# Kernel optimization log

Hardware: AMD Instinct MI355X
Metric: run time of the kernel (lower is better)

The kernel has to match this reference:

```python
import jax, jax.numpy as jnp
import numpy as np

EPS = 1e-6          # module eps for denominator
KERNEL_EPS = 1e-4   # performer softmax_kernel numerical eps


def softmax_kernel(data, projection):
    # data: [n, l, h, e]; projection: [m, e] -> features [n, l, h, m]
    d = data.shape[-1]
    m = projection.shape[0]
    data_normalizer = d ** -0.25
    ratio = m ** -0.5
    data_dash = jnp.einsum('nlhe,me->nlhm', data * data_normalizer, projection)
    diag_data = (0.5 * (data_normalizer ** 2)) * jnp.sum(data * data, axis=-1, keepdims=True)
    # numerically stable exp with per-row max subtraction
    data_dash = ratio * (jnp.exp(data_dash - diag_data - jnp.max(data_dash, axis=-1, keepdims=True)) + KERNEL_EPS)
    return data_dash


def _gaussian_orthogonal_random_matrix(nb_rows, nb_cols, seed=0):
    rng = np.random.default_rng(seed)
    blocks = []
    for _ in range(int(np.ceil(nb_rows / nb_cols))):
        q, _ = np.linalg.qr(rng.standard_normal((nb_cols, nb_cols)))
        blocks.append(q.T)
    proj = np.concatenate(blocks, axis=0)[:nb_rows]
    # scaling=0: chi-distributed row multipliers
    multiplier = np.linalg.norm(rng.standard_normal((nb_rows, nb_cols)), axis=1)
    return (multiplier[:, None] * proj).astype(np.float32)


def setup_inputs() -> dict:
    n, l, h, e = 2, 2048, 8, 64
    nb_features = l  # module: nb_features = l when l >= e
    key = jax.random.key(0)
    kq, kk, kv = jax.random.split(key, 3)
    queries = jax.random.normal(kq, (n, l, h, e), jnp.float32)
    keys = jax.random.normal(kk, (n, l, h, e), jnp.float32)
    values = jax.random.normal(kv, (n, l, h, e), jnp.float32)
    projection = jnp.asarray(_gaussian_orthogonal_random_matrix(nb_features, e))
    return {"queries": queries, "keys": keys, "values": values, "projection": projection}


def reference(queries, keys, values, projection):
    # Performer linear attention, batched (bi=None) branch
    q = softmax_kernel(queries, projection)   # [n, l, h, m]
    k = softmax_kernel(keys, projection)      # [n, l, h, m]
    kv = jnp.einsum('nshm,nshe->nhem', k, values)              # [n, h, e, m]
    z = 1.0 / (jnp.einsum('nlhm,nhm->nlh', q, k.sum(axis=1)) + EPS)  # [n, l, h]
    v = jnp.einsum('nlhm,nhem,nlh->nlhe', q, kv, z)             # [n, l, h, e]
    return v
```

## Files before the change

kernel.cpp:

```cpp
#include <hip/hip_runtime.h>


#define LL 2048
#define HH 8
#define MM 2048
#define ROWSTR 512

#define NORMC 0.35355339059327373f
#define LOG2E 1.4426950408889634f
#define NORMC2 (NORMC * LOG2E)
#define RATIO 0.022097086912079608f
#define KEPS 1e-4f
#define REPS (RATIO * KEPS)
#define EPSD 1e-6f

#define KVSPLIT 2097152
#define RSPLIT 32768

typedef __attribute__((ext_vector_type(8))) short short8;
typedef __attribute__((ext_vector_type(16))) float f32x16;

#define MFMA32(a, b, c) __builtin_amdgcn_mfma_f32_32x32x16_bf16((a), (b), (c), 0, 0, 0)

__device__ __forceinline__ void wg_barrier_lds() {
    asm volatile("s_waitcnt lgkmcnt(0)" ::: "memory");
    __builtin_amdgcn_s_barrier();
    __builtin_amdgcn_sched_barrier(0);
}

__device__ __forceinline__ f32x16 zero16() {
    f32x16 v;
    #pragma unroll
    for (int i = 0; i < 16; ++i) v[i] = 0.f;
    return v;
}
__device__ __forceinline__ unsigned short f2bf(float f) {
    union { float f; unsigned int u; } v; v.f = f;
    unsigned int r = v.u + 0x7fffu + ((v.u >> 16) & 1u);
    return (unsigned short)(r >> 16);
}
__device__ __forceinline__ unsigned int pk2(float lo, float hi) {
    return __builtin_amdgcn_perm(__float_as_uint(hi), __float_as_uint(lo), 0x07060302u);
}
__device__ __forceinline__ float bf2f(unsigned short u) {
    union { unsigned int ui; float f; } v; v.ui = ((unsigned int)u) << 16; return v.f;
}

template <bool BF16>
__device__ __forceinline__ short8 row_load8(const void* src, size_t rowbase, int off) {
    if (BF16) {
        return *(const short8*)((const unsigned short*)src + rowbase + off);
    } else {
        const float* p = (const float*)src + rowbase + off;
        float4 f0 = ((const float4*)p)[0], f1 = ((const float4*)p)[1];
        union { unsigned int u[4]; short8 s; } v;
        v.u[0] = pk2(f0.x, f0.y); v.u[1] = pk2(f0.z, f0.w);
        v.u[2] = pk2(f1.x, f1.y); v.u[3] = pk2(f1.z, f1.w);
        return v.s;
    }
}

template <bool BF16>
__device__ __forceinline__ void tile_load(const void* src, size_t base, size_t rstride,
                                          int t, uint4& A, uint4& B) {
    const int row = t >> 2, c16 = (t & 3) * 16;
    if (BF16) {
        const unsigned short* p = (const unsigned short*)src + base + (size_t)row * rstride + c16;
        A = *(const uint4*)p;
        B = *(const uint4*)(p + 8);
    } else {
        const float* p = (const float*)src + base + (size_t)row * rstride + c16;
        float4 f0 = ((const float4*)p)[0], f1 = ((const float4*)p)[1];
        float4 f2 = ((const float4*)p)[2], f3 = ((const float4*)p)[3];
        A.x = pk2(f0.x, f0.y); A.y = pk2(f0.z, f0.w);
        A.z = pk2(f1.x, f1.y); A.w = pk2(f1.z, f1.w);
        B.x = pk2(f2.x, f2.y); B.y = pk2(f2.z, f2.w);
        B.z = pk2(f3.x, f3.y); B.w = pk2(f3.z, f3.w);
    }
}
__device__ __forceinline__ void tile_store72(unsigned short* D, int t, uint4 A, uint4 B) {
    const int row = t >> 2, c16 = (t & 3) * 16;
    *(uint4*)&D[row * 72 + c16] = A;
    *(uint4*)&D[row * 72 + c16 + 8] = B;
}

template <bool BF16>
__device__ __forceinline__ void vt_load(const void* V, size_t base, int t, uint4& A, uint4& B) {
    const int s0 = (t & 31) * 2, e0 = (t >> 5) * 8;
    if (BF16) {
        const unsigned short* p = (const unsigned short*)V + base + (size_t)s0 * ROWSTR + e0;
        A = *(const uint4*)p;
        B = *(const uint4*)(p + ROWSTR);
    } else {
        const float* p = (const float*)V + base + (size_t)s0 * ROWSTR + e0;
        float4 f0 = ((const float4*)p)[0], f1 = ((const float4*)p)[1];
        const float* q = p + ROWSTR;
        float4 g0 = ((const float4*)q)[0], g1 = ((const float4*)q)[1];
        A.x = pk2(f0.x, f0.y); A.y = pk2(f0.z, f0.w);
        A.z = pk2(f1.x, f1.y); A.w = pk2(f1.z, f1.w);
        B.x = pk2(g0.x, g0.y); B.y = pk2(g0.z, g0.w);
        B.z = pk2(g1.x, g1.y); B.w = pk2(g1.z, g1.w);
    }
}
__device__ __forceinline__ void vt_store72(unsigned short* VT, int t, uint4 A, uint4 B) {
    const int s0 = (t & 31) * 2, e0 = (t >> 5) * 8;
    const unsigned ua[4] = {A.x, A.y, A.z, A.w}, ub[4] = {B.x, B.y, B.z, B.w};
    #pragma unroll
    for (int i = 0; i < 4; ++i) {
        *(unsigned*)&VT[(e0 + 2 * i) * 72 + s0] = (ua[i] & 0xFFFFu) | (ub[i] << 16);
        *(unsigned*)&VT[(e0 + 2 * i + 1) * 72 + s0] = (ua[i] >> 16) | (ub[i] & 0xFFFF0000u);
    }
}

__device__ __forceinline__ short8 xfrag(const unsigned int pd[8], int cp, int hi) {
    const unsigned int s0 = hi ? pd[4 * cp + 0] : pd[4 * cp + 2];
    const unsigned int s1 = hi ? pd[4 * cp + 1] : pd[4 * cp + 3];
    const unsigned int r0 = (unsigned int)__shfl_xor((int)s0, 32);
    const unsigned int r1 = (unsigned int)__shfl_xor((int)s1, 32);
    union { unsigned int u[4]; short8 s; } v;
    v.u[0] = hi ? r0 : pd[4 * cp + 0];
    v.u[1] = hi ? r1 : pd[4 * cp + 1];
    v.u[2] = hi ? pd[4 * cp + 2] : r0;
    v.u[3] = hi ? pd[4 * cp + 3] : r1;
    return v.s;
}

__global__ void LinearAttention_15985868276494_detect(const unsigned short* __restrict__ P,
                                                      float* __restrict__ flag) {
    if (threadIdx.x == 0) {
        int sane = 1;
        #pragma unroll
        for (int i = 0; i < 16; ++i) {
            const unsigned e = (P[2 * i] >> 7) & 0xFF;
            if (e < 101 || e > 141) sane = 0;
        }
        *flag = sane ? 1.0f : 0.0f;
    }
}

template <bool BF16>
__device__ void stats_impl(const void* X, const void* P, float* cws, char* smem) {
    unsigned short* Ps = (unsigned short*)smem;
    float* red = (float*)(smem + 18432);
    const int t = threadIdx.x;
    const int w = t >> 6, ln = t & 31, hi = (t >> 5) & 1;
    const int mstrip = w & 1, r3 = w >> 1;
    const int row_base = blockIdx.x * 128;
    const int ph = blockIdx.x & 31;

    short8 xb[4];
    #pragma unroll
    for (int c = 0; c < 4; ++c)
        xb[c] = row_load8<BF16>(X, (size_t)(row_base + r3 * 32 + ln) * 64, 16 * c + 8 * hi);

    const bool stP = (t < 256);
    const int tl = t & 255;
    uint4 pA, pB;
    if (stP) {
        uint4 a0, b0;
        tile_load<BF16>(P, (size_t)(ph * 64) * 64, 64, tl, a0, b0);
        tile_store72(Ps, tl, a0, b0);
        tile_load<BF16>(P, (size_t)(((ph + 1) & 31) * 64) * 64, 64, tl, pA, pB);
    }
    wg_barrier_lds();

    float rmax = -3e38f;
    for (int i = 0; i < 32; ++i) {
        const int cur = i & 1;
        unsigned short* Pc = Ps + cur * 4608;
        f32x16 acc = zero16();
        #pragma unroll
        for (int c = 0; c < 4; ++c) {
            const short8 af = *(const short8*)&Pc[(32 * mstrip + ln) * 72 + 16 * c + 8 * hi];
            acc = MFMA32(af, xb[c], acc);
        }
        if (stP && i + 1 < 32) {
            tile_store72(Ps + (cur ^ 1) * 4608, tl, pA, pB);
            if (i + 2 < 32)
                tile_load<BF16>(P, (size_t)(((i + 2 + ph) & 31) * 64) * 64, 64, tl, pA, pB);
        }
        #pragma unroll
        for (int r = 0; r < 16; ++r) rmax = fmaxf(rmax, acc[r]);
        wg_barrier_lds();
    }
    rmax = fmaxf(rmax, __shfl_xor(rmax, 32));
    if (hi == 0) red[w * 32 + ln] = rmax;
    float s2 = 0.f;
    if (mstrip == 0) {
        #pragma unroll
        for (int c = 0; c < 4; ++c) {
            union { short8 s; unsigned int u[4]; } uv; uv.s = xb[c];
            #pragma unroll
            for (int i2 = 0; i2 < 4; ++i2) {
                const float lo = bf2f((unsigned short)(uv.u[i2] & 0xFFFF));
                const float hv = bf2f((unsigned short)(uv.u[i2] >> 16));
                s2 = fmaf(lo, lo, s2); s2 = fmaf(hv, hv, s2);
            }
        }
        s2 += __shfl_xor(s2, 32);
    }
    wg_barrier_lds();
    if (mstrip == 0 && hi == 0) {
        const float rm = fmaxf(red[w * 32 + ln], red[(w + 1) * 32 + ln]);
        const int rg = row_base + r3 * 32 + ln;
        const int n = rg >> 14, l = (rg >> 3) & 2047, h = rg & 7;
        cws[(size_t)((n << 3) | h) * LL + l] =
            (NORMC * rm + (0.5f * NORMC * NORMC) * s2) * LOG2E;
    }
}

__global__ __launch_bounds__(512, 4) void LinearAttention_15985868276494_stats(
        const void* K, const void* Q, const void* P, const float* flag,
        float* c_k, float* c_q) {
    extern __shared__ char smem_st[];
    const void* X = (blockIdx.y == 0) ? K : Q;
    float* cws = (blockIdx.y == 0) ? c_k : c_q;
    if (*flag != 0.f) stats_impl<true>(X, P, cws, smem_st);
    else stats_impl<false>(X, P, cws, smem_st);
}

template <bool BF16>
__device__ void kv_impl(const void* K, const void* V, const void* P, const float* cws,
                        float* kvf01, float* ksum01, char* smem) {
    unsigned short* Ks = (unsigned short*)smem;
    unsigned short* VT = (unsigned short*)(smem + 18432);
    float* cks = (float*)(smem + 36864);

    const int t = threadIdx.x;
    const int w = t >> 6, ln = t & 31, hi = (t >> 5) & 1;
    const int mc = w;
    const int bid = blockIdx.x;
    const int xcd = bid & 7, rr = bid >> 3;
    const int gq = rr >> 3, mtb = rr & 7;
    const int g = gq * 8 + xcd;
    const int nh = g >> 2, sp = g & 3;
    const int n = nh >> 3, h = nh & 7;
    const size_t xbase = (size_t)n * (LL * ROWSTR) + (size_t)h * 64;
    const int st0 = sp * 8;
    const int mbase = mtb * 256;
    const int ph = mtb & 7;

    const bool stK = (t < 256);
    const int tl = t & 255;

    short8 pb[4];
    #pragma unroll
    for (int c = 0; c < 4; ++c)
        pb[c] = row_load8<BF16>(P, (size_t)(mbase + mc * 32 + ln) * 64, 16 * c + 8 * hi);

    uint4 kA, kB, vA, vB; float ckr = 0.f;
    {
        const int s_a = st0 + ph, s_b = st0 + ((ph + 1) & 7);
        if (stK) {
            tile_load<BF16>(K, xbase + (size_t)(s_a * 64) * ROWSTR, ROWSTR, tl, kA, kB);
            tile_store72(Ks, tl, kA, kB);
            tile_load<BF16>(K, xbase + (size_t)(s_b * 64) * ROWSTR, ROWSTR, tl, kA, kB);
        } else {
            vt_load<BF16>(V, xbase + (size_t)(s_a * 64) * ROWSTR, tl, vA, vB);
            vt_store72(VT, tl, vA, vB);
            vt_load<BF16>(V, xbase + (size_t)(s_b * 64) * ROWSTR, tl, vA, vB);
        }
        if (t < 64) {
            cks[t] = cws[(size_t)nh * LL + s_a * 64 + t];
            ckr = cws[(size_t)nh * LL + s_b * 64 + t];
        }
    }
    wg_barrier_lds();

    f32x16 akv0 = zero16(), akv1 = zero16();
    float ks = 0.f;

    for (int i = 0; i < 8; ++i) {
        const int cur = i & 1;
        unsigned short* Kc = Ks + cur * 4608;
        unsigned short* Vc = VT + cur * 4608;
        const float* cc = cks + cur * 64;
        #pragma unroll
        for (int ss = 0; ss < 2; ++ss) {
            f32x16 D = zero16();
            #pragma unroll
            for (int c = 0; c < 4; ++c) {
                const short8 af = *(const short8*)&Kc[(32 * ss + ln) * 72 + 16 * c + 8 * hi];
                D = MFMA32(af, pb[c], D);
            }
            if (ss == 0 && i + 1 < 8) {
                if (stK) tile_store72(Ks + (cur ^ 1) * 4608, tl, kA, kB);
                else vt_store72(VT + (cur ^ 1) * 4608, tl, vA, vB);
                if (t < 64) cks[(cur ^ 1) * 64 + t] = ckr;
                if (i + 2 < 8) {
                    const int st = st0 + ((i + 2 + ph) & 7);
                    if (stK) tile_load<BF16>(K, xbase + (size_t)(st * 64) * ROWSTR, ROWSTR, tl, kA, kB);
                    else vt_load<BF16>(V, xbase + (size_t)(st * 64) * ROWSTR, tl, vA, vB);
                    if (t < 64) ckr = cws[(size_t)nh * LL + st * 64 + t];
                }
            }
            unsigned int pd[8];
            #pragma unroll
            for (int gIdx = 0; gIdx < 4; ++gIdx) {
                const float4 c4 = *(const float4*)&cc[32 * ss + 8 * gIdx + 4 * hi];
                const float ca[4] = {c4.x, c4.y, c4.z, c4.w};
                float f[4];
                #pragma unroll
                for (int b = 0; b < 4; ++b) {
                    const float arg = fminf(fmaf(D[4 * gIdx + b], NORMC2, -ca[b]), 0.f);
                    f[b] = fmaf(__builtin_amdgcn_exp2f(arg), RATIO, REPS);
                }
                ks += (f[0] + f[1]) + (f[2] + f[3]);
                pd[2 * gIdx] = pk2(f[0], f[1]);
                pd[2 * gIdx + 1] = pk2(f[2], f[3]);
            }
            #pragma unroll
            for (int cp = 0; cp < 2; ++cp) {
                const short8 bf = xfrag(pd, cp, hi);
                const int scol = 32 * ss + 16 * cp + 8 * hi;
                const short8 v0 = *(const short8*)&Vc[ln * 72 + scol];
                const short8 v1 = *(const short8*)&Vc[(32 + ln) * 72 + scol];
                akv0 = MFMA32(v0, bf, akv0);
                akv1 = MFMA32(v1, bf, akv1);
            }
        }
        wg_barrier_lds();
    }
    {
        ks += __shfl_xor(ks, 32);
        const int m = mbase + mc * 32 + ln;
        if (hi == 0)
            ksum01[(size_t)sp * RSPLIT + (size_t)nh * MM + m] = ks;
        float* basep = kvf01 + (size_t)sp * KVSPLIT + (size_t)nh * (size_t)(64 * MM) + m;
        #pragma unroll
        for (int r = 0; r < 16; ++r) {
            const int e = (r & 3) + 8 * (r >> 2) + 4 * hi;
            basep[(size_t)e * MM] = akv0[r];
            basep[(size_t)(e + 32) * MM] = akv1[r];
        }
    }
}

__global__ __launch_bounds__(512, 4) void LinearAttention_15985868276494_kv(
        const void* K, const void* V, const void* P, const float* flag,
        const float* cws, float* kvf01, float* ksum01) {
    extern __shared__ char smem_kv[];
    if (*flag != 0.f) kv_impl<true>(K, V, P, cws, kvf01, ksum01, smem_kv);
    else kv_impl<false>(K, V, P, cws, kvf01, ksum01, smem_kv);
}

__global__ __launch_bounds__(256) void LinearAttention_15985868276494_reduce(
        const float* __restrict__ kvf01, const float* __restrict__ ksum01,
        unsigned short* __restrict__ kvT, float* __restrict__ ksumW) {
    const int gid = blockIdx.x * 256 + threadIdx.x;
    const size_t i4 = (size_t)gid * 4;
    const float4 a = *(const float4*)&kvf01[i4];
    const float4 b = *(const float4*)&kvf01[KVSPLIT + i4];
    const float4 c = *(const float4*)&kvf01[2 * (size_t)KVSPLIT + i4];
    const float4 d = *(const float4*)&kvf01[3 * (size_t)KVSPLIT + i4];
    uint2 o;
    o.x = (unsigned)f2bf(a.x + b.x + c.x + d.x) | ((unsigned)f2bf(a.y + b.y + c.y + d.y) << 16);
    o.y = (unsigned)f2bf(a.z + b.z + c.z + d.z) | ((unsigned)f2bf(a.w + b.w + c.w + d.w) << 16);
    *(uint2*)&kvT[i4] = o;
    if (blockIdx.x < 32) {
        const float4 e = *(const float4*)&ksum01[i4];
        const float4 f = *(const float4*)&ksum01[RSPLIT + i4];
        const float4 g = *(const float4*)&ksum01[2 * RSPLIT + i4];
        const float4 h = *(const float4*)&ksum01[3 * RSPLIT + i4];
        *(float4*)&ksumW[i4] = make_float4(e.x + f.x + g.x + h.x, e.y + f.y + g.y + h.y,
                                           e.z + f.z + g.z + h.z, e.w + f.w + g.w + h.w);
    }
}

template <bool BF16>
__device__ void out_impl(const void* Q, const void* P, const float* cqw,
                         const unsigned short* kvT, const float* ksum,
                         float* po, float* pad, char* smem) {
    unsigned short* Ps = (unsigned short*)smem;
    unsigned short* KVs = (unsigned short*)(smem + 18432);
    unsigned short* kss = (unsigned short*)(smem + 36864);
    float* fin = (float*)smem;

    const int t = threadIdx.x;
    const int w = t >> 6, ln = t & 31, hi = (t >> 5) & 1;
    const int lc = w & 3, mspl = w >> 2;
    const int bid = blockIdx.x;
    const int xcd = bid & 7, rr = bid >> 3;
    const int gq = rr >> 4, lbb = rr & 15;
    const int g = gq * 8 + xcd;
    const int nh = g >> 1, sp = g & 1;
    const int n = nh >> 3, h = nh & 7;
    const size_t qbase = (size_t)n * (LL * ROWSTR) + (size_t)h * 64;
    const size_t kvbase = (size_t)nh * (size_t)(64 * MM);
    const int mt0 = sp * 16;
    const int lbase = lbb * 128;
    const int ph = lbb;

    const bool stP = (t < 256);
    const int tl = t & 255;

    short8 qb[4];
    #pragma unroll
    for (int c = 0; c < 4; ++c)
        qb[c] = row_load8<BF16>(Q, qbase + (size_t)(lbase + lc * 32 + ln) * ROWSTR, 16 * c + 8 * hi);
    const float cq = cqw[(size_t)nh * LL + lbase + lc * 32 + ln];

    uint4 pA, pB, kA, kB; float ksr = 0.f;
    {
        const int m_a = mt0 + (ph & 15), m_b = mt0 + ((ph + 1) & 15);
        if (stP) {
            tile_load<BF16>(P, (size_t)(m_a * 64) * 64, 64, tl, pA, pB);
            tile_store72(Ps, tl, pA, pB);
            tile_load<BF16>(P, (size_t)(m_b * 64) * 64, 64, tl, pA, pB);
        } else {
            tile_load<true>(kvT, kvbase + m_a * 64, MM, tl, kA, kB);
            tile_store72(KVs, tl, kA, kB);
            tile_load<true>(kvT, kvbase + m_b * 64, MM, tl, kA, kB);
        }
        if (t < 64) {
            kss[t] = f2bf(ksum[(size_t)nh * MM + m_a * 64 + t]);
            ksr = ksum[(size_t)nh * MM + m_b * 64 + t];
        }
    }
    wg_barrier_lds();

    f32x16 ao0 = zero16(), ao1 = zero16(), ad = zero16();

    for (int i = 0; i < 16; ++i) {
        const int cur = i & 1;
        unsigned short* Pc = Ps + cur * 4608;
        unsigned short* Kc = KVs + cur * 4608;
        const unsigned short* ksc = kss + cur * 64;
        f32x16 D = zero16();
        #pragma unroll
        for (int c = 0; c < 4; ++c) {
            const short8 af = *(const short8*)&Pc[(32 * mspl + ln) * 72 + 16 * c + 8 * hi];
            D = MFMA32(af, qb[c], D);
        }
        if (i + 1 < 16) {
            if (stP) tile_store72(Ps + (cur ^ 1) * 4608, tl, pA, pB);
            else tile_store72(KVs + (cur ^ 1) * 4608, tl, kA, kB);
            if (t < 64) kss[(cur ^ 1) * 64 + t] = f2bf(ksr);
            if (i + 2 < 16) {
                const int mt = mt0 + ((i + 2 + ph) & 15);
                if (stP) tile_load<BF16>(P, (size_t)(mt * 64) * 64, 64, tl, pA, pB);
                else tile_load<true>(kvT, kvbase + mt * 64, MM, tl, kA, kB);
                if (t < 64) ksr = ksum[(size_t)nh * MM + mt * 64 + t];
            }
        }
        unsigned int pd[8];
        #pragma unroll
        for (int gIdx = 0; gIdx < 4; ++gIdx) {
            float f[4];
            #pragma unroll
            for (int b = 0; b < 4; ++b) {
                const float arg = fminf(fmaf(D[4 * gIdx + b], NORMC2, -cq), 0.f);
                f[b] = fmaf(__builtin_amdgcn_exp2f(arg), RATIO, REPS);
            }
            pd[2 * gIdx] = pk2(f[0], f[1]);
            pd[2 * gIdx + 1] = pk2(f[2], f[3]);
        }
        #pragma unroll
        for (int cp = 0; cp < 2; ++cp) {
            const short8 bf = xfrag(pd, cp, hi);
            const int mcol = 32 * mspl + 16 * cp + 8 * hi;
            const short8 a0 = *(const short8*)&Kc[ln * 72 + mcol];
            const short8 a1 = *(const short8*)&Kc[(32 + ln) * 72 + mcol];
            const short8 k8 = *(const short8*)&ksc[mcol];
            ao0 = MFMA32(a0, bf, ao0);
            ao1 = MFMA32(a1, bf, ao1);
            ad = MFMA32(k8, bf, ad);
        }
        wg_barrier_lds();
    }
    #pragma unroll 1
    for (int e2 = 0; e2 < 2; ++e2) {
        if ((lc >> 1) == e2) {
            const int slot = ((lc & 1) * 2 + mspl);
            const int addr = (slot * 64 + (t & 63)) * 33;
            #pragma unroll
            for (int r = 0; r < 16; ++r) fin[addr + r] = ao0[r];
            #pragma unroll
            for (int r = 0; r < 16; ++r) fin[addr + 16 + r] = ao1[r];
            fin[addr + 32] = ad[0];
        }
        wg_barrier_lds();
        {
            const int l64 = t >> 3, eg = t & 7;
            const int lcl = l64 >> 5, lane_l = l64 & 31;
            const int s0 = (lcl * 2) * 64, s1 = (lcl * 2 + 1) * 64;
            const float adt = fin[(s0 + lane_l) * 33 + 32] + fin[(s1 + lane_l) * 33 + 32];
            const int l = lbase + (e2 * 2 + lcl) * 32 + lane_l;
            const size_t row = (size_t)(n * LL + l) * HH + h;
            if (eg == 0) pad[(size_t)sp * RSPLIT + row] = adt;
            float* dst = po + (size_t)sp * KVSPLIT + row * 64 + eg * 8;
            #pragma unroll
            for (int jq = 0; jq < 2; ++jq) {
                float o[4];
                #pragma unroll
                for (int b = 0; b < 4; ++b) {
                    const int e = eg * 8 + 4 * jq + b;
                    const int t16 = e >> 5, e5 = e & 31;
                    const int hi_s = (e5 >> 2) & 1;
                    const int reg = 16 * t16 + (e5 & 3) + 4 * (e5 >> 3);
                    const int lane_s = hi_s * 32 + lane_l;
                    o[b] = fin[(s0 + lane_s) * 33 + reg] + fin[(s1 + lane_s) * 33 + reg];
                }
                *(float4*)&dst[4 * jq] = make_float4(o[0], o[1], o[2], o[3]);
            }
        }
        wg_barrier_lds();
    }
}

__global__ __launch_bounds__(512, 4) void LinearAttention_15985868276494_out(
        const void* Q, const void* P, const float* flag, const float* cqw,
        const unsigned short* kvT, const float* ksum, float* po, float* pad) {
    extern __shared__ char smem_out[];
    if (*flag != 0.f) out_impl<true>(Q, P, cqw, kvT, ksum, po, pad, smem_out);
    else out_impl<false>(Q, P, cqw, kvT, ksum, po, pad, smem_out);
}

__global__ __launch_bounds__(256) void LinearAttention_15985868276494_out2(
        const float* __restrict__ po, const float* __restrict__ pad,
        const float* __restrict__ flag, void* __restrict__ outp) {
    const int gid = blockIdx.x * 256 + threadIdx.x;
    const int row = gid >> 2, eg = gid & 3;
    const float adt = pad[row] + pad[RSPLIT + row];
    const float z = 1.0f / (adt + EPSD);
    const size_t base = (size_t)row * 64 + eg * 16;
    float vals[16];
    #pragma unroll
    for (int q4 = 0; q4 < 4; ++q4) {
        const float4 a = *(const float4*)&po[base + 4 * q4];
        const float4 b = *(const float4*)&po[KVSPLIT + base + 4 * q4];
        vals[4 * q4 + 0] = (a.x + b.x) * z;
        vals[4 * q4 + 1] = (a.y + b.y) * z;
        vals[4 * q4 + 2] = (a.z + b.z) * z;
        vals[4 * q4 + 3] = (a.w + b.w) * z;
    }
    if (*flag != 0.f) {
        uint4 o0, o1;
        o0.x = (unsigned)f2bf(vals[0]) | ((unsigned)f2bf(vals[1]) << 16);
        o0.y = (unsigned)f2bf(vals[2]) | ((unsigned)f2bf(vals[3]) << 16);
        o0.z = (unsigned)f2bf(vals[4]) | ((unsigned)f2bf(vals[5]) << 16);
        o0.w = (unsigned)f2bf(vals[6]) | ((unsigned)f2bf(vals[7]) << 16);
        o1.x = (unsigned)f2bf(vals[8]) | ((unsigned)f2bf(vals[9]) << 16);
        o1.y = (unsigned)f2bf(vals[10]) | ((unsigned)f2bf(vals[11]) << 16);
        o1.z = (unsigned)f2bf(vals[12]) | ((unsigned)f2bf(vals[13]) << 16);
        o1.w = (unsigned)f2bf(vals[14]) | ((unsigned)f2bf(vals[15]) << 16);
        unsigned short* op = (unsigned short*)outp + base;
        *(uint4*)op = o0;
        *(uint4*)(op + 8) = o1;
    } else {
        float* op = (float*)outp + base;
        #pragma unroll
        for (int q4 = 0; q4 < 4; ++q4)
            *(float4*)&op[4 * q4] = make_float4(vals[4 * q4], vals[4 * q4 + 1],
                                                vals[4 * q4 + 2], vals[4 * q4 + 3]);
    }
}

extern "C" void kernel_launch(void* const* d_in, const int* in_sizes, int n_in,
                              void* d_out, int out_size, void* d_ws, size_t ws_size,
                              hipStream_t stream) {
    const void* Q = d_in[0];
    const void* K = d_in[1];
    const void* V = d_in[2];
    const void* P = d_in[3];

    float* W = (float*)d_ws;
    float* flag = W;
    float* c_k = W + 16;
    float* c_q = c_k + 32768;
    float* ksum01 = c_q + 32768;
    float* kvf01 = ksum01 + 4 * RSPLIT;
    float* ksumW = kvf01 + 4 * (size_t)KVSPLIT;
    unsigned short* kvTW = (unsigned short*)(ksumW + RSPLIT);

    LinearAttention_15985868276494_detect<<<1, 64, 0, stream>>>(
        (const unsigned short*)P, flag);
    LinearAttention_15985868276494_stats<<<dim3(256, 2), 512, 19456, stream>>>(
        K, Q, P, flag, c_k, c_q);
    LinearAttention_15985868276494_kv<<<dim3(512), 512, 37376, stream>>>(
        K, V, P, flag, c_k, kvf01, ksum01);
    LinearAttention_15985868276494_reduce<<<2048, 256, 0, stream>>>(
        kvf01, ksum01, kvTW, ksumW);
    LinearAttention_15985868276494_out<<<dim3(512), 512, 37120, stream>>>(
        Q, P, flag, c_q, kvTW, ksumW, kvf01, ksum01);
    LinearAttention_15985868276494_out2<<<512, 256, 0, stream>>>(
        kvf01, ksum01, flag, d_out);
}
```

Measured before the change: 180.6 us.

## Software-pipeline the feature-projection MFMA one step ahead with triple-buffered tiles

In the kv and out kernels, the projection MFMA for the next sub-tile is now issued before the exp and second-GEMM work of the current sub-tile, so the two MFMA chains can overlap. The K and P tiles move to a three-slot LDS ring, which lets the next tile be read while the tile after it is being stored. This raises LDS use per block from about 37 KB to about 46 KB and adds live registers for the extra accumulator, which may lower occupancy.

```diff
diff --git a/kernel.cpp b/kernel.cpp
--- a/kernel.cpp
+++ b/kernel.cpp
@@ -223,8 +223,8 @@
 __device__ void kv_impl(const void* K, const void* V, const void* P, const float* cws,
                         float* kvf01, float* ksum01, char* smem) {
     unsigned short* Ks = (unsigned short*)smem;
-    unsigned short* VT = (unsigned short*)(smem + 18432);
-    float* cks = (float*)(smem + 36864);
+    unsigned short* VT = (unsigned short*)(smem + 27648);
+    float* cks = (float*)(smem + 46080);
 
     const int t = threadIdx.x;
     const int w = t >> 6, ln = t & 31, hi = (t >> 5) & 1;
@@ -250,48 +250,73 @@
 
     uint4 kA, kB, vA, vB; float ckr = 0.f;
     {
-        const int s_a = st0 + ph, s_b = st0 + ((ph + 1) & 7);
+        const int s0i = st0 + (ph & 7);
+        const int s1i = st0 + ((ph + 1) & 7);
+        const int s2i = st0 + ((ph + 2) & 7);
         if (stK) {
-            tile_load<BF16>(K, xbase + (size_t)(s_a * 64) * ROWSTR, ROWSTR, tl, kA, kB);
+            tile_load<BF16>(K, xbase + (size_t)(s0i * 64) * ROWSTR, ROWSTR, tl, kA, kB);
             tile_store72(Ks, tl, kA, kB);
-            tile_load<BF16>(K, xbase + (size_t)(s_b * 64) * ROWSTR, ROWSTR, tl, kA, kB);
+            tile_load<BF16>(K, xbase + (size_t)(s1i * 64) * ROWSTR, ROWSTR, tl, kA, kB);
+            tile_store72(Ks + 4608, tl, kA, kB);
+            tile_load<BF16>(K, xbase + (size_t)(s2i * 64) * ROWSTR, ROWSTR, tl, kA, kB);
         } else {
-            vt_load<BF16>(V, xbase + (size_t)(s_a * 64) * ROWSTR, tl, vA, vB);
+            vt_load<BF16>(V, xbase + (size_t)(s0i * 64) * ROWSTR, tl, vA, vB);
             vt_store72(VT, tl, vA, vB);
-            vt_load<BF16>(V, xbase + (size_t)(s_b * 64) * ROWSTR, tl, vA, vB);
+            vt_load<BF16>(V, xbase + (size_t)(s1i * 64) * ROWSTR, tl, vA, vB);
         }
         if (t < 64) {
-            cks[t] = cws[(size_t)nh * LL + s_a * 64 + t];
-            ckr = cws[(size_t)nh * LL + s_b * 64 + t];
+            cks[t] = cws[(size_t)nh * LL + s0i * 64 + t];
+            ckr = cws[(size_t)nh * LL + s1i * 64 + t];
         }
     }
     wg_barrier_lds();
+
+    f32x16 D = zero16();
+    #pragma unroll
+    for (int c = 0; c < 4; ++c) {
+        const short8 af = *(const short8*)&Ks[ln * 72 + 16 * c + 8 * hi];
+        D = MFMA32(af, pb[c], D);
+    }
 
     f32x16 akv0 = zero16(), akv1 = zero16();
     float ks = 0.f;
 
     for (int i = 0; i < 8; ++i) {
-        const int cur = i & 1;
-        unsigned short* Kc = Ks + cur * 4608;
-        unsigned short* Vc = VT + cur * 4608;
-        const float* cc = cks + cur * 64;
+        unsigned short* Vc = VT + (i & 1) * 4608;
+        const float* cc = cks + (i & 1) * 64;
         #pragma unroll
         for (int ss = 0; ss < 2; ++ss) {
-            f32x16 D = zero16();
-            #pragma unroll
-            for (int c = 0; c < 4; ++c) {
-                const short8 af = *(const short8*)&Kc[(32 * ss + ln) * 72 + 16 * c + 8 * hi];
-                D = MFMA32(af, pb[c], D);
+            f32x16 Dn = zero16();
+            const int jn = 2 * i + ss + 1;
+            if (jn < 16) {
+                const int tn = jn >> 1, ssn = jn & 1;
+                unsigned short* Kc = Ks + (tn % 3) * 4608;
+                #pragma unroll
+                for (int c = 0; c < 4; ++c) {
+                    const short8 af = *(const short8*)&Kc[(32 * ssn + ln) * 72 + 16 * c + 8 * hi];
+                    Dn = MFMA32(af, pb[c], Dn);
+                }
             }
             if (ss == 0 && i + 1 < 8) {
-                if (stK) tile_store72(Ks + (cur ^ 1) * 4608, tl, kA, kB);
-                else vt_store72(VT + (cur ^ 1) * 4608, tl, vA, vB);
-                if (t < 64) cks[(cur ^ 1) * 64 + t] = ckr;
-                if (i + 2 < 8) {
-                    const int st = st0 + ((i + 2 + ph) & 7);
-                    if (stK) tile_load<BF16>(K, xbase + (size_t)(st * 64) * ROWSTR, ROWSTR, tl, kA, kB);
-                    else vt_load<BF16>(V, xbase + (size_t)(st * 64) * ROWSTR, tl, vA, vB);
-                    if (t < 64) ckr = cws[(size_t)nh * LL + st * 64 + t];
+                if (stK) {
+                    if (i + 2 < 8) tile_store72(Ks + ((i + 2) % 3) * 4608, tl, kA, kB);
+                    if (i + 3 < 8) {
+                        const int st = st0 + ((i + 3 + ph) & 7);
+                        tile_load<BF16>(K, xbase + (size_t)(st * 64) * ROWSTR, ROWSTR, tl, kA, kB);
+                    }
+                } else {
+                    vt_store72(VT + ((i + 1) & 1) * 4608, tl, vA, vB);
+                    if (i + 2 < 8) {
+                        const int st = st0 + ((i + 2 + ph) & 7);
+                        vt_load<BF16>(V, xbase + (size_t)(st * 64) * ROWSTR, tl, vA, vB);
+                    }
+                }
+                if (t < 64) {
+                    cks[((i + 1) & 1) * 64 + t] = ckr;
+                    if (i + 2 < 8) {
+                        const int st = st0 + ((i + 2 + ph) & 7);
+                        ckr = cws[(size_t)nh * LL + st * 64 + t];
+                    }
                 }
             }
             unsigned int pd[8];
@@ -318,6 +343,7 @@
                 akv0 = MFMA32(v0, bf, akv0);
                 akv1 = MFMA32(v1, bf, akv1);
             }
+            D = Dn;
         }
         wg_barrier_lds();
     }
@@ -372,8 +398,8 @@
                          const unsigned short* kvT, const float* ksum,
                          float* po, float* pad, char* smem) {
     unsigned short* Ps = (unsigned short*)smem;
-    unsigned short* KVs = (unsigned short*)(smem + 18432);
-    unsigned short* kss = (unsigned short*)(smem + 36864);
+    unsigned short* KVs = (unsigned short*)(smem + 27648);
+    unsigned short* kss = (unsigned short*)(smem + 46080);
     float* fin = (float*)smem;
 
     const int t = threadIdx.x;
@@ -402,45 +428,66 @@
 
     uint4 pA, pB, kA, kB; float ksr = 0.f;
     {
-        const int m_a = mt0 + (ph & 15), m_b = mt0 + ((ph + 1) & 15);
+        const int m0i = mt0 + (ph & 15);
+        const int m1i = mt0 + ((ph + 1) & 15);
+        const int m2i = mt0 + ((ph + 2) & 15);
         if (stP) {
-            tile_load<BF16>(P, (size_t)(m_a * 64) * 64, 64, tl, pA, pB);
+            tile_load<BF16>(P, (size_t)(m0i * 64) * 64, 64, tl, pA, pB);
             tile_store72(Ps, tl, pA, pB);
-            tile_load<BF16>(P, (size_t)(m_b * 64) * 64, 64, tl, pA, pB);
+            tile_load<BF16>(P, (size_t)(m1i * 64) * 64, 64, tl, pA, pB);
+            tile_store72(Ps + 4608, tl, pA, pB);
+            tile_load<BF16>(P, (size_t)(m2i * 64) * 64, 64, tl, pA, pB);
         } else {
-            tile_load<true>(kvT, kvbase + m_a * 64, MM, tl, kA, kB);
+            tile_load<true>(kvT, kvbase + m0i * 64, MM, tl, kA, kB);
             tile_store72(KVs, tl, kA, kB);
-            tile_load<true>(kvT, kvbase + m_b * 64, MM, tl, kA, kB);
+            tile_load<true>(kvT, kvbase + m1i * 64, MM, tl, kA, kB);
         }
         if (t < 64) {
-            kss[t] = f2bf(ksum[(size_t)nh * MM + m_a * 64 + t]);
-            ksr = ksum[(size_t)nh * MM + m_b * 64 + t];
+            kss[t] = f2bf(ksum[(size_t)nh * MM + m0i * 64 + t]);
+            ksr = ksum[(size_t)nh * MM + m1i * 64 + t];
         }
     }
     wg_barrier_lds();
 
+    f32x16 D = zero16();
+    #pragma unroll
+    for (int c = 0; c < 4; ++c) {
+        const short8 af = *(const short8*)&Ps[(32 * mspl + ln) * 72 + 16 * c + 8 * hi];
+        D = MFMA32(af, qb[c], D);
+    }
+
     f32x16 ao0 = zero16(), ao1 = zero16(), ad = zero16();
 
     for (int i = 0; i < 16; ++i) {
-        const int cur = i & 1;
-        unsigned short* Pc = Ps + cur * 4608;
-        unsigned short* Kc = KVs + cur * 4608;
-        const unsigned short* ksc = kss + cur * 64;
-        f32x16 D = zero16();
-        #pragma unroll
-        for (int c = 0; c < 4; ++c) {
-            const short8 af = *(const short8*)&Pc[(32 * mspl + ln) * 72 + 16 * c + 8 * hi];
-            D = MFMA32(af, qb[c], D);
-        }
+        f32x16 Dn = zero16();
         if (i + 1 < 16) {
-            if (stP) tile_store72(Ps + (cur ^ 1) * 4608, tl, pA, pB);
-            else tile_store72(KVs + (cur ^ 1) * 4608, tl, kA, kB);
-            if (t < 64) kss[(cur ^ 1) * 64 + t] = f2bf(ksr);
-            if (i + 2 < 16) {
-                const int mt = mt0 + ((i + 2 + ph) & 15);
-                if (stP) tile_load<BF16>(P, (size_t)(mt * 64) * 64, 64, tl, pA, pB);
-                else tile_load<true>(kvT, kvbase + mt * 64, MM, tl, kA, kB);
-                if (t < 64) ksr = ksum[(size_t)nh * MM + mt * 64 + t];
+            unsigned short* Pc = Ps + ((i + 1) % 3) * 4608;
+            #pragma unroll
+            for (int c = 0; c < 4; ++c) {
+                const short8 af = *(const short8*)&Pc[(32 * mspl + ln) * 72 + 16 * c + 8 * hi];
+                Dn = MFMA32(af, qb[c], Dn);
+            }
+        }
+        if (i + 1 < 16) {
+            if (stP) {
+                if (i + 2 < 16) tile_store72(Ps + ((i + 2) % 3) * 4608, tl, pA, pB);
+                if (i + 3 < 16) {
+                    const int mt = mt0 + ((i + 3 + ph) & 15);
+                    tile_load<BF16>(P, (size_t)(mt * 64) * 64, 64, tl, pA, pB);
+                }
+            } else {
+                tile_store72(KVs + ((i + 1) & 1) * 4608, tl, kA, kB);
+                if (i + 2 < 16) {
+                    const int mt = mt0 + ((i + 2 + ph) & 15);
+                    tile_load<true>(kvT, kvbase + mt * 64, MM, tl, kA, kB);
+                }
+            }
+            if (t < 64) {
+                kss[((i + 1) & 1) * 64 + t] = f2bf(ksr);
+                if (i + 2 < 16) {
+                    const int mt = mt0 + ((i + 2 + ph) & 15);
+                    ksr = ksum[(size_t)nh * MM + mt * 64 + t];
+                }
             }
         }
         unsigned int pd[8];
@@ -455,17 +502,22 @@
             pd[2 * gIdx] = pk2(f[0], f[1]);
             pd[2 * gIdx + 1] = pk2(f[2], f[3]);
         }
-        #pragma unroll
-        for (int cp = 0; cp < 2; ++cp) {
-            const short8 bf = xfrag(pd, cp, hi);
-            const int mcol = 32 * mspl + 16 * cp + 8 * hi;
-            const short8 a0 = *(const short8*)&Kc[ln * 72 + mcol];
-            const short8 a1 = *(const short8*)&Kc[(32 + ln) * 72 + mcol];
-            const short8 k8 = *(const short8*)&ksc[mcol];
-            ao0 = MFMA32(a0, bf, ao0);
-            ao1 = MFMA32(a1, bf, ao1);
-            ad = MFMA32(k8, bf, ad);
-        }
+        {
+            unsigned short* Kc = KVs + (i & 1) * 4608;
+            const unsigned short* ksc = kss + (i & 1) * 64;
+            #pragma unroll
+            for (int cp = 0; cp < 2; ++cp) {
+                const short8 bf = xfrag(pd, cp, hi);
+                const int mcol = 32 * mspl + 16 * cp + 8 * hi;
+                const short8 a0 = *(const short8*)&Kc[ln * 72 + mcol];
+                const short8 a1 = *(const short8*)&Kc[(32 + ln) * 72 + mcol];
+                const short8 k8 = *(const short8*)&ksc[mcol];
+                ao0 = MFMA32(a0, bf, ao0);
+                ao1 = MFMA32(a1, bf, ao1);
+                ad = MFMA32(k8, bf, ad);
+            }
+        }
+        D = Dn;
         wg_barrier_lds();
     }
     #pragma unroll 1
@@ -577,11 +629,11 @@
         (const unsigned short*)P, flag);
     LinearAttention_15985868276494_stats<<<dim3(256, 2), 512, 19456, stream>>>(
         K, Q, P, flag, c_k, c_q);
-    LinearAttention_15985868276494_kv<<<dim3(512), 512, 37376, stream>>>(
+    LinearAttention_15985868276494_kv<<<dim3(512), 512, 46592, stream>>>(
         K, V, P, flag, c_k, kvf01, ksum01);
     LinearAttention_15985868276494_reduce<<<2048, 256, 0, stream>>>(
         kvf01, ksum01, kvTW, ksumW);
-    LinearAttention_15985868276494_out<<<dim3(512), 512, 37120, stream>>>(
+    LinearAttention_15985868276494_out<<<dim3(512), 512, 46336, stream>>>(
         Q, P, flag, c_q, kvTW, ksumW, kvf01, ksum01);
     LinearAttention_15985868276494_out2<<<512, 256, 0, stream>>>(
         kvf01, ksum01, flag, d_out);
```

New measurement: 205.1 us. +13.6%, slower.

## Fuse out2 normalization into out kernel by dropping the m-split

Applied to the files above, without the earlier changes.

The output kernel no longer splits the feature dimension across two blocks and writes fp32 partials. Each block now covers 64 rows of l over all 2048 features, processing two 64-wide feature tiles per iteration. Waves are split four ways across tile-half and m-half, and the partials are reduced in LDS. The normalization and bf16/fp32 store are done in-kernel, which removes the out2 launch and the partial-buffer round trip through global memory. In exchange, LDS use per block doubles to about 74 KB, which may lower occupancy, and each block does more serial work.

```diff
diff --git a/kernel.cpp b/kernel.cpp
--- a/kernel.cpp
+++ b/kernel.cpp
@@ -370,26 +370,24 @@
 template <bool BF16>
 __device__ void out_impl(const void* Q, const void* P, const float* cqw,
                          const unsigned short* kvT, const float* ksum,
-                         float* po, float* pad, char* smem) {
+                         void* outp, char* smem) {
     unsigned short* Ps = (unsigned short*)smem;
-    unsigned short* KVs = (unsigned short*)(smem + 18432);
-    unsigned short* kss = (unsigned short*)(smem + 36864);
+    unsigned short* KVs = (unsigned short*)(smem + 36864);
+    unsigned short* kss = (unsigned short*)(smem + 73728);
     float* fin = (float*)smem;
 
     const int t = threadIdx.x;
     const int w = t >> 6, ln = t & 31, hi = (t >> 5) & 1;
-    const int lc = w & 3, mspl = w >> 2;
+    const int lc = w & 1, mspl = (w >> 1) & 1, ts = w >> 2;
     const int bid = blockIdx.x;
     const int xcd = bid & 7, rr = bid >> 3;
-    const int gq = rr >> 4, lbb = rr & 15;
-    const int g = gq * 8 + xcd;
-    const int nh = g >> 1, sp = g & 1;
+    const int nh = xcd | ((rr & 1) << 3);
+    const int lbb = rr >> 1;
     const int n = nh >> 3, h = nh & 7;
     const size_t qbase = (size_t)n * (LL * ROWSTR) + (size_t)h * 64;
     const size_t kvbase = (size_t)nh * (size_t)(64 * MM);
-    const int mt0 = sp * 16;
-    const int lbase = lbb * 128;
-    const int ph = lbb;
+    const int lbase = lbb * 64;
+    const int ph = lbb & 15;
 
     const bool stP = (t < 256);
     const int tl = t & 255;
@@ -400,21 +398,27 @@
         qb[c] = row_load8<BF16>(Q, qbase + (size_t)(lbase + lc * 32 + ln) * ROWSTR, 16 * c + 8 * hi);
     const float cq = cqw[(size_t)nh * LL + lbase + lc * 32 + ln];
 
-    uint4 pA, pB, kA, kB; float ksr = 0.f;
+    uint4 eA, eB, oA, oB; float ksr = 0.f;
     {
-        const int m_a = mt0 + (ph & 15), m_b = mt0 + ((ph + 1) & 15);
+        const int p0 = ph, p1 = (ph + 1) & 15;
         if (stP) {
-            tile_load<BF16>(P, (size_t)(m_a * 64) * 64, 64, tl, pA, pB);
-            tile_store72(Ps, tl, pA, pB);
-            tile_load<BF16>(P, (size_t)(m_b * 64) * 64, 64, tl, pA, pB);
+            tile_load<BF16>(P, (size_t)(p0 * 128) * 64, 64, tl, eA, eB);
+            tile_store72(Ps, tl, eA, eB);
+            tile_load<BF16>(P, (size_t)(p0 * 128 + 64) * 64, 64, tl, eA, eB);
+            tile_store72(Ps + 4608, tl, eA, eB);
+            tile_load<BF16>(P, (size_t)(p1 * 128) * 64, 64, tl, eA, eB);
+            tile_load<BF16>(P, (size_t)(p1 * 128 + 64) * 64, 64, tl, oA, oB);
         } else {
-            tile_load<true>(kvT, kvbase + m_a * 64, MM, tl, kA, kB);
-            tile_store72(KVs, tl, kA, kB);
-            tile_load<true>(kvT, kvbase + m_b * 64, MM, tl, kA, kB);
-        }
-        if (t < 64) {
-            kss[t] = f2bf(ksum[(size_t)nh * MM + m_a * 64 + t]);
-            ksr = ksum[(size_t)nh * MM + m_b * 64 + t];
+            tile_load<true>(kvT, kvbase + p0 * 128, MM, tl, eA, eB);
+            tile_store72(KVs, tl, eA, eB);
+            tile_load<true>(kvT, kvbase + p0 * 128 + 64, MM, tl, eA, eB);
+            tile_store72(KVs + 4608, tl, eA, eB);
+            tile_load<true>(kvT, kvbase + p1 * 128, MM, tl, eA, eB);
+            tile_load<true>(kvT, kvbase + p1 * 128 + 64, MM, tl, oA, oB);
+        }
+        if (t < 128) {
+            kss[t] = f2bf(ksum[(size_t)nh * MM + p0 * 128 + t]);
+            ksr = ksum[(size_t)nh * MM + p1 * 128 + t];
         }
     }
     wg_barrier_lds();
@@ -423,9 +427,9 @@
 
     for (int i = 0; i < 16; ++i) {
         const int cur = i & 1;
-        unsigned short* Pc = Ps + cur * 4608;
-        unsigned short* Kc = KVs + cur * 4608;
-        const unsigned short* ksc = kss + cur * 64;
+        unsigned short* Pc = Ps + cur * 9216 + ts * 4608;
+        unsigned short* Kc = KVs + cur * 9216 + ts * 4608;
+        const unsigned short* ksc = kss + cur * 128 + ts * 64;
         f32x16 D = zero16();
         #pragma unroll
         for (int c = 0; c < 4; ++c) {
@@ -433,14 +437,29 @@
             D = MFMA32(af, qb[c], D);
         }
         if (i + 1 < 16) {
-            if (stP) tile_store72(Ps + (cur ^ 1) * 4608, tl, pA, pB);
-            else tile_store72(KVs + (cur ^ 1) * 4608, tl, kA, kB);
-            if (t < 64) kss[(cur ^ 1) * 64 + t] = f2bf(ksr);
-            if (i + 2 < 16) {
-                const int mt = mt0 + ((i + 2 + ph) & 15);
-                if (stP) tile_load<BF16>(P, (size_t)(mt * 64) * 64, 64, tl, pA, pB);
-                else tile_load<true>(kvT, kvbase + mt * 64, MM, tl, kA, kB);
-                if (t < 64) ksr = ksum[(size_t)nh * MM + mt * 64 + t];
+            if (stP) {
+                tile_store72(Ps + (cur ^ 1) * 9216, tl, eA, eB);
+                tile_store72(Ps + (cur ^ 1) * 9216 + 4608, tl, oA, oB);
+                if (i + 2 < 16) {
+                    const int p = (i + 2 + ph) & 15;
+                    tile_load<BF16>(P, (size_t)(p * 128) * 64, 64, tl, eA, eB);
+                    tile_load<BF16>(P, (size_t)(p * 128 + 64) * 64, 64, tl, oA, oB);
+                }
+            } else {
+                tile_store72(KVs + (cur ^ 1) * 9216, tl, eA, eB);
+                tile_store72(KVs + (cur ^ 1) * 9216 + 4608, tl, oA, oB);
+                if (i + 2 < 16) {
+                    const int p = (i + 2 + ph) & 15;
+                    tile_load<true>(kvT, kvbase + p * 128, MM, tl, eA, eB);
+                    tile_load<true>(kvT, kvbase + p * 128 + 64, MM, tl, oA, oB);
+                }
+            }
+            if (t < 128) {
+                kss[(cur ^ 1) * 128 + t] = f2bf(ksr);
+                if (i + 2 < 16) {
+                    const int p = (i + 2 + ph) & 15;
+                    ksr = ksum[(size_t)nh * MM + p * 128 + t];
+                }
             }
         }
         unsigned int pd[8];
@@ -470,9 +489,8 @@
     }
     #pragma unroll 1
     for (int e2 = 0; e2 < 2; ++e2) {
-        if ((lc >> 1) == e2) {
-            const int slot = ((lc & 1) * 2 + mspl);
-            const int addr = (slot * 64 + (t & 63)) * 33;
+        if (lc == e2) {
+            const int addr = ((mspl * 2 + ts) * 64 + (t & 63)) * 33;
             #pragma unroll
             for (int r = 0; r < 16; ++r) fin[addr + r] = ao0[r];
             #pragma unroll
@@ -481,27 +499,35 @@
         }
         wg_barrier_lds();
         {
-            const int l64 = t >> 3, eg = t & 7;
-            const int lcl = l64 >> 5, lane_l = l64 & 31;
-            const int s0 = (lcl * 2) * 64, s1 = (lcl * 2 + 1) * 64;
-            const float adt = fin[(s0 + lane_l) * 33 + 32] + fin[(s1 + lane_l) * 33 + 32];
-            const int l = lbase + (e2 * 2 + lcl) * 32 + lane_l;
+            const int l32 = t >> 4, eg = t & 15;
+            const int lane_l = l32;
+            float adt = 0.f;
+            #pragma unroll
+            for (int s = 0; s < 4; ++s) adt += fin[(s * 64 + lane_l) * 33 + 32];
+            const float z = 1.0f / (adt + EPSD);
+            const int l = lbase + e2 * 32 + l32;
             const size_t row = (size_t)(n * LL + l) * HH + h;
-            if (eg == 0) pad[(size_t)sp * RSPLIT + row] = adt;
-            float* dst = po + (size_t)sp * KVSPLIT + row * 64 + eg * 8;
-            #pragma unroll
-            for (int jq = 0; jq < 2; ++jq) {
-                float o[4];
+            float vals[4];
+            #pragma unroll
+            for (int b = 0; b < 4; ++b) {
+                const int e = eg * 4 + b;
+                const int t16 = e >> 5, e5 = e & 31;
+                const int hi_s = (e5 >> 2) & 1;
+                const int reg = 16 * t16 + (e5 & 3) + 4 * (e5 >> 3);
+                const int lane_s = hi_s * 32 + lane_l;
+                float o = 0.f;
                 #pragma unroll
-                for (int b = 0; b < 4; ++b) {
-                    const int e = eg * 8 + 4 * jq + b;
-                    const int t16 = e >> 5, e5 = e & 31;
-                    const int hi_s = (e5 >> 2) & 1;
-                    const int reg = 16 * t16 + (e5 & 3) + 4 * (e5 >> 3);
-                    const int lane_s = hi_s * 32 + lane_l;
-                    o[b] = fin[(s0 + lane_s) * 33 + reg] + fin[(s1 + lane_s) * 33 + reg];
-                }
-                *(float4*)&dst[4 * jq] = make_float4(o[0], o[1], o[2], o[3]);
+                for (int s = 0; s < 4; ++s) o += fin[(s * 64 + lane_s) * 33 + reg];
+                vals[b] = o * z;
+            }
+            if (BF16) {
+                uint2 ov;
+                ov.x = (unsigned)f2bf(vals[0]) | ((unsigned)f2bf(vals[1]) << 16);
+                ov.y = (unsigned)f2bf(vals[2]) | ((unsigned)f2bf(vals[3]) << 16);
+                *(uint2*)((unsigned short*)outp + row * 64 + eg * 4) = ov;
+            } else {
+                *(float4*)((float*)outp + row * 64 + eg * 4) =
+                    make_float4(vals[0], vals[1], vals[2], vals[3]);
             }
         }
         wg_barrier_lds();
@@ -510,50 +536,10 @@
 
 __global__ __launch_bounds__(512, 4) void LinearAttention_15985868276494_out(
         const void* Q, const void* P, const float* flag, const float* cqw,
-        const unsigned short* kvT, const float* ksum, float* po, float* pad) {
+        const unsigned short* kvT, const float* ksum, void* outp) {
     extern __shared__ char smem_out[];
-    if (*flag != 0.f) out_impl<true>(Q, P, cqw, kvT, ksum, po, pad, smem_out);
-    else out_impl<false>(Q, P, cqw, kvT, ksum, po, pad, smem_out);
-}
-
-__global__ __launch_bounds__(256) void LinearAttention_15985868276494_out2(
-        const float* __restrict__ po, const float* __restrict__ pad,
-        const float* __restrict__ flag, void* __restrict__ outp) {
-    const int gid = blockIdx.x * 256 + threadIdx.x;
-    const int row = gid >> 2, eg = gid & 3;
-    const float adt = pad[row] + pad[RSPLIT + row];
-    const float z = 1.0f / (adt + EPSD);
-    const size_t base = (size_t)row * 64 + eg * 16;
-    float vals[16];
-    #pragma unroll
-    for (int q4 = 0; q4 < 4; ++q4) {
-        const float4 a = *(const float4*)&po[base + 4 * q4];
-        const float4 b = *(const float4*)&po[KVSPLIT + base + 4 * q4];
-        vals[4 * q4 + 0] = (a.x + b.x) * z;
-        vals[4 * q4 + 1] = (a.y + b.y) * z;
-        vals[4 * q4 + 2] = (a.z + b.z) * z;
-        vals[4 * q4 + 3] = (a.w + b.w) * z;
-    }
-    if (*flag != 0.f) {
-        uint4 o0, o1;
-        o0.x = (unsigned)f2bf(vals[0]) | ((unsigned)f2bf(vals[1]) << 16);
-        o0.y = (unsigned)f2bf(vals[2]) | ((unsigned)f2bf(vals[3]) << 16);
-        o0.z = (unsigned)f2bf(vals[4]) | ((unsigned)f2bf(vals[5]) << 16);
-        o0.w = (unsigned)f2bf(vals[6]) | ((unsigned)f2bf(vals[7]) << 16);
-        o1.x = (unsigned)f2bf(vals[8]) | ((unsigned)f2bf(vals[9]) << 16);
-        o1.y = (unsigned)f2bf(vals[10]) | ((unsigned)f2bf(vals[11]) << 16);
-        o1.z = (unsigned)f2bf(vals[12]) | ((unsigned)f2bf(vals[13]) << 16);
-        o1.w = (unsigned)f2bf(vals[14]) | ((unsigned)f2bf(vals[15]) << 16);
-        unsigned short* op = (unsigned short*)outp + base;
-        *(uint4*)op = o0;
-        *(uint4*)(op + 8) = o1;
-    } else {
-        float* op = (float*)outp + base;
-        #pragma unroll
-        for (int q4 = 0; q4 < 4; ++q4)
-            *(float4*)&op[4 * q4] = make_float4(vals[4 * q4], vals[4 * q4 + 1],
-                                                vals[4 * q4 + 2], vals[4 * q4 + 3]);
-    }
+    if (*flag != 0.f) out_impl<true>(Q, P, cqw, kvT, ksum, outp, smem_out);
+    else out_impl<false>(Q, P, cqw, kvT, ksum, outp, smem_out);
 }
 
 extern "C" void kernel_launch(void* const* d_in, const int* in_sizes, int n_in,
@@ -581,8 +567,6 @@
         K, V, P, flag, c_k, kvf01, ksum01);
     LinearAttention_15985868276494_reduce<<<2048, 256, 0, stream>>>(
         kvf01, ksum01, kvTW, ksumW);
-    LinearAttention_15985868276494_out<<<dim3(512), 512, 37120, stream>>>(
-        Q, P, flag, c_q, kvTW, ksumW, kvf01, ksum01);
-    LinearAttention_15985868276494_out2<<<512, 256, 0, stream>>>(
-        kvf01, ksum01, flag, d_out);
-}
+    LinearAttention_15985868276494_out<<<dim3(512), 512, 74240, stream>>>(
+        Q, P, flag, c_q, kvTW, ksumW, d_out);
+}
```

Result: faster. 176.8 us (median of 2 runs) (-2.1%).
